# Kernel optimization log

Measured on AMD Instinct MI355X. Metric: run time of the kernel, lower is better.

The kernel has to match this reference:

```python
import jax, jax.numpy as jnp
import numpy as np
from jax import lax

B, C, H, W = 16, 256, 128, 128
MAX_ROOMS = 10

def _conv(x, w, b):
    y = lax.conv_general_dilated(x, w, window_strides=(1, 1), padding='SAME',
                                 dimension_numbers=('NCHW', 'OIHW', 'NCHW'))
    return y + b[None, :, None, None]

def setup_inputs() -> dict:
    key = jax.random.key(0)
    ks = jax.random.split(key, 16)
    def w(k, shape, fan_in):
        return jax.random.normal(k, shape, jnp.float32) * (1.0 / np.sqrt(fan_in))
    inp = {
        'features': jax.random.normal(ks[0], (B, C, H, W), jnp.float32),
        'conv1_w': w(ks[1], (C // 2, C, 3, 3), C * 9),
        'conv1_b': jnp.zeros((C // 2,), jnp.float32),
        'conv2_w': w(ks[2], (MAX_ROOMS, C // 2, 3, 3), (C // 2) * 9),
        'conv2_b': jnp.zeros((MAX_ROOMS,), jnp.float32),
        'lin1_w': w(ks[3], (256, C * 64), C * 64),
        'lin1_b': jnp.zeros((256,), jnp.float32),
        'lin2_w': w(ks[4], (128, 256), 256),
        'lin2_b': jnp.zeros((128,), jnp.float32),
        'adj1_w': w(ks[5], (64, 256), 256),
        'adj1_b': jnp.zeros((64,), jnp.float32),
        'adj2_w': w(ks[6], (32, 64), 64),
        'adj2_b': jnp.zeros((32,), jnp.float32),
        'adj3_w': w(ks[7], (1, 32), 32),
        'adj3_b': jnp.zeros((1,), jnp.float32),
    }
    return inp

def reference(features, conv1_w, conv1_b, conv2_w, conv2_b,
              lin1_w, lin1_b, lin2_w, lin2_b,
              adj1_w, adj1_b, adj2_w, adj2_b, adj3_w, adj3_b):
    # room detector: conv -> relu -> conv -> sigmoid
    h = jax.nn.relu(_conv(features, conv1_w, conv1_b))
    room_maps = jax.nn.sigmoid(_conv(h, conv2_w, conv2_b))  # [B, max_rooms, H, W]

    # room features: adaptive avg pool to 8x8 (exact since H,W divisible by 8)
    b, c = features.shape[0], features.shape[1]
    pooled = features.reshape(b, c, 8, H // 8, 8, W // 8).mean(axis=(3, 5))  # [B,C,8,8]
    flat = pooled.reshape(b, c * 64)
    feat = jax.nn.relu(flat @ lin1_w.T + lin1_b) @ lin2_w.T + lin2_b  # [B,128]

    # adjacency: original loop uses the SAME pair_feat=cat([feat,feat]) for every (i,j),
    # so compute one prob per batch row and broadcast to all off-diagonal entries.
    pair = jnp.concatenate([feat, feat], axis=-1)  # [B,256]
    a = jax.nn.relu(pair @ adj1_w.T + adj1_b)
    a = jax.nn.relu(a @ adj2_w.T + adj2_b)
    p = jax.nn.sigmoid(a @ adj3_w.T + adj3_b)  # [B,1]
    off_diag = 1.0 - jnp.eye(MAX_ROOMS, dtype=features.dtype)
    adjacency = p[:, :, None] * off_diag[None]  # [B, max_rooms, max_rooms]

    return room_maps, feat, adjacency
```

## Files before the change

### kernel.cpp

```cpp
#include <hip/hip_runtime.h>

#define HH 128
#define WW 128
#define FEAT_OFF 2621440ull
#define ADJ_OFF  2623488ull

typedef __bf16 bf16x8 __attribute__((ext_vector_type(8)));
typedef float  f32x4  __attribute__((ext_vector_type(4)));
typedef float  f32x16 __attribute__((ext_vector_type(16)));

__device__ __forceinline__ unsigned short f2bf(float f) {
  unsigned int u = __float_as_uint(f);
  unsigned int r = ((u >> 16) & 1u) + 0x7fffu;
  return (unsigned short)((u + r) >> 16);
}
__device__ __forceinline__ void gl_lds16(const void* g, void* l) {
  __builtin_amdgcn_global_load_lds((const __attribute__((address_space(1))) unsigned int*)g,
                                   (__attribute__((address_space(3))) unsigned int*)l, 16, 0, 0);
}
__device__ __forceinline__ int SW(int r) { return (r ^ (r >> 2)) & 3; }

#define FENCE() asm volatile("" ::: "memory")
#define BARRIER() do { FENCE(); __builtin_amdgcn_s_barrier(); FENCE(); } while (0)
#define LBAR() do { asm volatile("s_waitcnt lgkmcnt(0)" ::: "memory"); __builtin_amdgcn_s_barrier(); FENCE(); } while (0)

__global__ void prep_kernel(const float* __restrict__ w1, const float* __restrict__ w2,
                            unsigned short* __restrict__ W1t, unsigned short* __restrict__ W2t,
                            unsigned short* __restrict__ zp) {
  int id = blockIdx.x * 256 + threadIdx.x;
  if (id < 2048) zp[id] = 0;
  if (id < 294912) {
    int ci = id & 255, co = (id >> 8) & 127, dxy = id >> 15;
    int dy = dxy / 3, dx = dxy - 3 * dy;
    W1t[id] = f2bf(w1[((co * 256 + ci) * 3 + dy) * 3 + dx]);
  }
  if (id < 18432) {
    int ci = id & 127, co = (id >> 7) & 15, dxy = id >> 11;
    int dy = dxy / 3, dx = dxy - 3 * dy;
    W2t[id] = (co < 10) ? f2bf(w2[((co * 128 + ci) * 3 + dy) * 3 + dx]) : (unsigned short)0;
  }
}

__global__ void nhwc_kernel(const float* __restrict__ F, unsigned short* __restrict__ Xn,
                            float* __restrict__ part) {
  __shared__ __align__(16) unsigned short tile[16384];
  __shared__ float pl[1024];
  int t = threadIdx.x, bi = blockIdx.x;
  int chalf = bi & 1, y = (bi >> 1) & 127, b = bi >> 8;
  int c0 = chalf * 128;
  int cp = t >> 2, xq = t & 3;
  const float* rowA = F + (((size_t)(b * 256 + c0 + cp * 2)) * HH + y) * WW + xq * 32;
  const float* rowB = rowA + (size_t)HH * WW;
  unsigned int* tw = (unsigned int*)tile;
  float s00 = 0.f, s01 = 0.f, s10 = 0.f, s11 = 0.f;
#pragma unroll
  for (int jj = 0; jj < 8; ++jj) {
    float4 va = *(const float4*)(rowA + jj * 4);
    float4 vb = *(const float4*)(rowB + jj * 4);
    float av[4] = {va.x, va.y, va.z, va.w};
    float bv[4] = {vb.x, vb.y, vb.z, vb.w};
#pragma unroll
    for (int e = 0; e < 4; ++e) {
      int xl = jj * 4 + e;
      int x = xq * 32 + xl;
      if (xl < 16) { s00 += av[e]; s10 += bv[e]; } else { s01 += av[e]; s11 += bv[e]; }
      unsigned int word = (unsigned int)f2bf(av[e]) | ((unsigned int)f2bf(bv[e]) << 16);
      tw[x * 64 + (((cp >> 2) ^ (x & 15)) << 2) + (cp & 3)] = word;
    }
  }
  pl[(cp * 2 + 0) * 8 + xq * 2 + 0] = s00;
  pl[(cp * 2 + 0) * 8 + xq * 2 + 1] = s01;
  pl[(cp * 2 + 1) * 8 + xq * 2 + 0] = s10;
  pl[(cp * 2 + 1) * 8 + xq * 2 + 1] = s11;
  __syncthreads();
  int x = t >> 1, h = t & 1;
  unsigned short* dst = Xn + ((((size_t)b * HH + y) * WW) + x) * 256 + c0;
#pragma unroll
  for (int k = 0; k < 8; ++k) {
    int s = h * 8 + k;
    *(uint4*)(dst + s * 8) = *(const uint4*)(tile + x * 128 + ((s ^ (x & 15)) << 3));
  }
  *(float4*)&part[((((size_t)b * 128 + y) * 2) + chalf) * 1024 + t * 4] = *(const float4*)&pl[t * 4];
}

__global__ void pool3_kernel(const float* __restrict__ part, float* __restrict__ pooled) {
  int bi = blockIdx.x, t = threadIdx.x;
  int py = bi & 7, chalf = (bi >> 3) & 1, b = bi >> 4;
#pragma unroll
  for (int q = 0; q < 4; ++q) {
    int i = q * 256 + t;
    float s = 0.f;
#pragma unroll
    for (int yy = 0; yy < 16; ++yy)
      s += part[((((size_t)b * 128 + py * 16 + yy) * 2) + chalf) * 1024 + i];
    int ch = i >> 3, px = i & 7;
    pooled[(size_t)b * 16384 + (chalf * 128 + ch) * 64 + py * 8 + px] = s * (1.f / 256.f);
  }
}

__global__ __launch_bounds__(512) void conv1_kernel(const unsigned short* __restrict__ X,
                                                    const unsigned short* __restrict__ Wt,
                                                    const float* __restrict__ bias,
                                                    unsigned short* __restrict__ Hout,
                                                    const unsigned short* __restrict__ zp) {
  extern __shared__ __align__(16) unsigned short smem[];
  const int t = threadIdx.x, l = t & 63, w = t >> 6;
  int bid = (blockIdx.x & 7) * 64 + (blockIdx.x >> 3);
  const int b = bid >> 5, y0 = (bid & 31) * 4;
  const int lane31 = l & 31, lh = l >> 5;
  const int yloc = w >> 1, xh = w & 1, xoff = xh * 64;

  f32x16 acc[2][4];
#pragma unroll
  for (int i = 0; i < 2; ++i)
#pragma unroll
    for (int j = 0; j < 4; ++j)
#pragma unroll
      for (int e = 0; e < 16; ++e) acc[i][j][e] = 0.f;

  auto issue_group = [&](int p, int i0, int i1, int bufsel) {
    int dy = p >> 3, cb = p & 7;
    unsigned short* buf = smem + bufsel * 30720;
    for (int i = i0; i < i1; ++i) {
      int c = w + 8 * i;
      if (c >= 60) break;
      const unsigned short* g;
      if (c < 36) {
        int air = c / 9, jj = c - air * 9;
        int er = jj * 16 + (l >> 2);
        int xin = er - 1;
        int row = y0 - 1 + dy + air;
        if (row >= 0 && row < HH && xin >= 0 && xin < WW && er < 130) {
          int kq = (l & 3) ^ SW(er);
          g = X + (((size_t)b * HH + row) * WW + xin) * 256 + cb * 32 + kq * 8;
        } else g = zp + l * 8;
      } else {
        int cc = c - 36;
        int dxi = cc >> 3, jj = cc & 7;
        int co = jj * 16 + (l >> 2);
        int kq = (l & 3) ^ SW(co);
        g = Wt + (((size_t)(dy * 3 + dxi)) * 128 + co) * 256 + cb * 32 + kq * 8;
      }
      gl_lds16(g, buf + c * 512);
    }
  };

  issue_group(0, 0, 8, 0);

  for (int p = 0; p < 24; ++p) {
    const unsigned short* buf = smem + (p & 1) * 30720;
    const unsigned short* Ab = buf + yloc * 4608;
    const unsigned short* Bb = buf + 18432;
    const int nsel = (p + 1) & 1;

    if (p < 23) issue_group(p + 1, 0, 3, nsel);
    FENCE();
    if (p < 23) asm volatile("s_waitcnt vmcnt(3)" ::: "memory");
    else        asm volatile("s_waitcnt vmcnt(0)" ::: "memory");
    BARRIER();

#pragma unroll
    for (int dx = 0; dx < 3; ++dx) {
      if (p < 23) {
        if (dx == 1)      issue_group(p + 1, 3, 6, nsel);
        else if (dx == 2) issue_group(p + 1, 6, 8, nsel);
      }
      bf16x8 a[2][2], bb[4][2];
#pragma unroll
      for (int tm = 0; tm < 2; ++tm)
#pragma unroll
        for (int ks = 0; ks < 2; ++ks) {
          int er = xoff + tm * 32 + lane31 + dx;
          int slot = (ks * 2 + lh) ^ SW(er);
          a[tm][ks] = *(const bf16x8*)(Ab + er * 32 + slot * 8);
        }
#pragma unroll
      for (int tn = 0; tn < 4; ++tn)
#pragma unroll
        for (int ks = 0; ks < 2; ++ks) {
          int co = tn * 32 + lane31;
          int slot = (ks * 2 + lh) ^ SW(co);
          bb[tn][ks] = *(const bf16x8*)(Bb + dx * 4096 + co * 32 + slot * 8);
        }
      __builtin_amdgcn_s_setprio(1);
#pragma unroll
      for (int ks = 0; ks < 2; ++ks)
#pragma unroll
        for (int tm = 0; tm < 2; ++tm)
#pragma unroll
          for (int tn = 0; tn < 4; ++tn)
            acc[tm][tn] = __builtin_amdgcn_mfma_f32_32x32x16_bf16(a[tm][ks], bb[tn][ks], acc[tm][tn], 0, 0, 0);
      __builtin_amdgcn_s_setprio(0);
    }
    BARRIER();
  }

  unsigned short* E = smem;
  for (int r = 0; r < 2; ++r) {
    if (xh == r) {
#pragma unroll
      for (int tn = 0; tn < 4; ++tn) {
        int co = tn * 32 + lane31;
        float bv = bias[co];
#pragma unroll
        for (int tm = 0; tm < 2; ++tm)
#pragma unroll
          for (int rr = 0; rr < 16; ++rr) {
            int row = (rr & 3) + 8 * (rr >> 2) + 4 * lh;
            int xl = tm * 32 + row;
            E[yloc * 8704 + xl * 136 + co] = f2bf(fmaxf(acc[tm][tn][rr] + bv, 0.f));
          }
      }
    }
    LBAR();
#pragma unroll
    for (int k = 0; k < 8; ++k) {
      int idx = k * 512 + t;
      int yl = idx >> 10, rem = idx & 1023;
      int xl = rem >> 4, oct = rem & 15;
      const uint4 v = *(const uint4*)(E + yl * 8704 + xl * 136 + oct * 8);
      size_t g = (((size_t)b * HH + y0 + yl) * WW + r * 64 + xl) * 128 + oct * 8;
      *(uint4*)(Hout + g) = v;
    }
    LBAR();
  }
}

__global__ __launch_bounds__(256) void conv2_kernel(const unsigned short* __restrict__ Hn,
                                                    const unsigned short* __restrict__ Wt,
                                                    const float* __restrict__ bias,
                                                    float* __restrict__ rmaps,
                                                    const unsigned short* __restrict__ zp) {
  extern __shared__ __align__(16) unsigned short smem[];
  const int t = threadIdx.x, l = t & 63, w = t >> 6;
  int bid = (blockIdx.x & 7) * 64 + (blockIdx.x >> 3);
  const int b = bid >> 5, y0 = (bid & 31) * 4;
  const int ko = l >> 4, r0 = l & 15;
  const int yloc = w;

  f32x4 acc[8];
#pragma unroll
  for (int i = 0; i < 8; ++i) acc[i] = {0.f, 0.f, 0.f, 0.f};

  auto stage = [&](int cb, int bufsel) {
    unsigned short* buf = smem + bufsel * 32256;
    for (int c = w; c < 63; c += 4) {
      const unsigned short* g;
      if (c < 54) {
        int air = c / 9, jj = c - air * 9;
        int er = jj * 16 + (l >> 2);
        int xin = er - 1;
        int row = y0 - 1 + air;
        if (row >= 0 && row < HH && xin >= 0 && xin < WW && er < 130) {
          int kq = (l & 3) ^ SW(er);
          g = Hn + (((size_t)b * HH + row) * WW + xin) * 128 + cb * 32 + kq * 8;
        } else g = zp + l * 8;
      } else {
        int tap = c - 54;
        int co = l >> 2;
        int kq = (l & 3) ^ SW(co);
        g = Wt + ((size_t)tap * 16 + co) * 128 + cb * 32 + kq * 8;
      }
      gl_lds16(g, buf + c * 512);
    }
  };

  stage(0, 0);
  for (int p = 0; p < 4; ++p) {
    if (p < 3) {
      stage(p + 1, (p + 1) & 1);
      FENCE();
      asm volatile("s_waitcnt vmcnt(15)" ::: "memory");
    } else {
      FENCE();
      asm volatile("s_waitcnt vmcnt(0)" ::: "memory");
    }
    BARRIER();
    const unsigned short* buf = smem + (p & 1) * 32256;
#pragma unroll
    for (int dy = 0; dy < 3; ++dy) {
      const unsigned short* Ab = buf + (yloc + dy) * 4608;
#pragma unroll
      for (int dx = 0; dx < 3; ++dx) {
        int tap = dy * 3 + dx;
        bf16x8 bbf = *(const bf16x8*)(buf + (54 + tap) * 512 + r0 * 32 + ((ko ^ SW(r0)) << 3));
        __builtin_amdgcn_s_setprio(1);
#pragma unroll
        for (int mf = 0; mf < 8; ++mf) {
          int er = mf * 16 + r0 + dx;
          bf16x8 a = *(const bf16x8*)(Ab + er * 32 + ((ko ^ SW(er)) << 3));
          acc[mf] = __builtin_amdgcn_mfma_f32_16x16x32_bf16(a, bbf, acc[mf], 0, 0, 0);
        }
        __builtin_amdgcn_s_setprio(0);
      }
    }
    BARRIER();
  }

  int co = r0;
  if (co < 10) {
    float bv = bias[co];
    int y = y0 + yloc;
#pragma unroll
    for (int mf = 0; mf < 8; ++mf) {
      int x = mf * 16 + ko * 4;
      float4 o;
      o.x = 1.f / (1.f + __expf(-(acc[mf][0] + bv)));
      o.y = 1.f / (1.f + __expf(-(acc[mf][1] + bv)));
      o.z = 1.f / (1.f + __expf(-(acc[mf][2] + bv)));
      o.w = 1.f / (1.f + __expf(-(acc[mf][3] + bv)));
      *(float4*)&rmaps[(((size_t)b * 10 + co) * HH + y) * WW + x] = o;
    }
  }
}

__global__ void lin1_kernel(const float* __restrict__ pooled, const float* __restrict__ w1,
                            const float* __restrict__ b1, float* __restrict__ hidden) {
  int o = blockIdx.x, t = threadIdx.x;
  float acc[16];
#pragma unroll
  for (int b = 0; b < 16; ++b) acc[b] = 0.f;
  const float* wr = w1 + (size_t)o * 16384;
  for (int i = t; i < 16384; i += 256) {
    float wv = wr[i];
#pragma unroll
    for (int b = 0; b < 16; ++b) acc[b] += wv * pooled[(size_t)b * 16384 + i];
  }
  __shared__ float red[16][4];
#pragma unroll
  for (int b = 0; b < 16; ++b) {
    float v = acc[b];
    for (int s = 32; s; s >>= 1) v += __shfl_down(v, s);
    if ((t & 63) == 0) red[b][t >> 6] = v;
  }
  __syncthreads();
  if (t < 16) {
    float v = red[t][0] + red[t][1] + red[t][2] + red[t][3] + b1[o];
    hidden[o * 16 + t] = fmaxf(v, 0.f);
  }
}

__global__ void head_kernel(const float* __restrict__ hidden,
                            const float* __restrict__ w2, const float* __restrict__ b2,
                            const float* __restrict__ a1w, const float* __restrict__ a1b,
                            const float* __restrict__ a2w, const float* __restrict__ a2b,
                            const float* __restrict__ a3w, const float* __restrict__ a3b,
                            float* __restrict__ out) {
  int b = blockIdx.x, t = threadIdx.x;
  __shared__ float hid[256], fs[128], a1[64], a2[32], pv;
  hid[t] = hidden[t * 16 + b];
  __syncthreads();
  if (t < 128) {
    float s = b2[t];
    for (int k = 0; k < 256; ++k) s += hid[k] * w2[t * 256 + k];
    fs[t] = s;
    out[FEAT_OFF + b * 128 + t] = s;
  }
  __syncthreads();
  if (t < 64) {
    float s = a1b[t];
    for (int k = 0; k < 128; ++k) s += fs[k] * (a1w[t * 256 + k] + a1w[t * 256 + 128 + k]);
    a1[t] = fmaxf(s, 0.f);
  }
  __syncthreads();
  if (t < 32) {
    float s = a2b[t];
    for (int k = 0; k < 64; ++k) s += a1[k] * a2w[t * 64 + k];
    a2[t] = fmaxf(s, 0.f);
  }
  __syncthreads();
  if (t == 0) {
    float s = a3b[0];
    for (int k = 0; k < 32; ++k) s += a2[k] * a3w[k];
    pv = 1.f / (1.f + __expf(-s));
  }
  __syncthreads();
  if (t < 100) out[ADJ_OFF + b * 100 + t] = ((t / 10) == (t % 10)) ? 0.f : pv;
}

extern "C" void kernel_launch(void* const* d_in, const int* in_sizes, int n_in,
                              void* d_out, int out_size, void* d_ws, size_t ws_size,
                              hipStream_t stream) {
  const float* F   = (const float*)d_in[0];
  const float* w1  = (const float*)d_in[1];
  const float* b1  = (const float*)d_in[2];
  const float* w2  = (const float*)d_in[3];
  const float* b2  = (const float*)d_in[4];
  const float* l1w = (const float*)d_in[5];
  const float* l1b = (const float*)d_in[6];
  const float* l2w = (const float*)d_in[7];
  const float* l2b = (const float*)d_in[8];
  const float* a1w = (const float*)d_in[9];
  const float* a1b = (const float*)d_in[10];
  const float* a2w = (const float*)d_in[11];
  const float* a2b = (const float*)d_in[12];
  const float* a3w = (const float*)d_in[13];
  const float* a3b = (const float*)d_in[14];
  float* out = (float*)d_out;
  char* ws = (char*)d_ws;

  const size_t zp_off   = 0;
  const size_t w1t_off  = 4096;
  const size_t w2t_off  = w1t_off + 589824;
  const size_t xn_off   = w2t_off + 36864;
  const size_t hn_off   = xn_off + 134217728ull;
  const size_t pool_off = hn_off + 67108864ull;
  const size_t hid_off  = pool_off + 1048576ull;
  const size_t need     = hid_off + 16384ull;
  if (ws_size < need) return;

  unsigned short* zp  = (unsigned short*)(ws + zp_off);
  unsigned short* W1t = (unsigned short*)(ws + w1t_off);
  unsigned short* W2t = (unsigned short*)(ws + w2t_off);
  unsigned short* Xn  = (unsigned short*)(ws + xn_off);
  unsigned short* Hn  = (unsigned short*)(ws + hn_off);
  float* part   = (float*)(ws + hn_off);
  float* pooled = (float*)(ws + pool_off);
  float* hidden = (float*)(ws + hid_off);

  hipFuncSetAttribute((const void*)conv1_kernel, hipFuncAttributeMaxDynamicSharedMemorySize, 122880);
  hipFuncSetAttribute((const void*)conv2_kernel, hipFuncAttributeMaxDynamicSharedMemorySize, 129024);

  prep_kernel<<<1152, 256, 0, stream>>>(w1, w2, W1t, W2t, zp);
  nhwc_kernel<<<4096, 256, 0, stream>>>(F, Xn, part);
  pool3_kernel<<<256, 256, 0, stream>>>(part, pooled);
  conv1_kernel<<<512, 512, 122880, stream>>>(Xn, W1t, b1, Hn, zp);
  conv2_kernel<<<512, 256, 129024, stream>>>(Hn, W2t, b2, out, zp);
  lin1_kernel<<<256, 256, 0, stream>>>(pooled, l1w, l1b, hidden);
  head_kernel<<<16, 256, 0, stream>>>(hidden, l2w, l2b, a1w, a1b, a2w, a2b, a3w, a3b, out);
}
```

Baseline: 367.1 us.

## Fuse weight prep into NHWC kernel, transpose pooled for lin1, tweak conv2 waits

Folds the weight-conversion prep kernel into the first 1152 blocks of the NHWC transpose kernel, removing one launch. The pool kernel also writes a batch-minor transposed copy of the pooled features, so lin1 can read 16 batch values as contiguous float4 vectors and load the weights as float4. In conv2, the wait count is split per wave and the s_setprio hints around the MFMA loop are removed. This adds an extra pooled buffer write and puts prep work on a few transpose blocks, which may slightly unbalance them.

```diff
diff --git a/kernel.cpp b/kernel.cpp
--- a/kernel.cpp
+++ b/kernel.cpp
@@ -24,28 +24,28 @@
 #define BARRIER() do { FENCE(); __builtin_amdgcn_s_barrier(); FENCE(); } while (0)
 #define LBAR() do { asm volatile("s_waitcnt lgkmcnt(0)" ::: "memory"); __builtin_amdgcn_s_barrier(); FENCE(); } while (0)
 
-__global__ void prep_kernel(const float* __restrict__ w1, const float* __restrict__ w2,
+__global__ void nhwc_kernel(const float* __restrict__ F, unsigned short* __restrict__ Xn,
+                            float* __restrict__ part,
+                            const float* __restrict__ w1, const float* __restrict__ w2,
                             unsigned short* __restrict__ W1t, unsigned short* __restrict__ W2t,
                             unsigned short* __restrict__ zp) {
-  int id = blockIdx.x * 256 + threadIdx.x;
-  if (id < 2048) zp[id] = 0;
-  if (id < 294912) {
-    int ci = id & 255, co = (id >> 8) & 127, dxy = id >> 15;
-    int dy = dxy / 3, dx = dxy - 3 * dy;
-    W1t[id] = f2bf(w1[((co * 256 + ci) * 3 + dy) * 3 + dx]);
-  }
-  if (id < 18432) {
-    int ci = id & 127, co = (id >> 7) & 15, dxy = id >> 11;
-    int dy = dxy / 3, dx = dxy - 3 * dy;
-    W2t[id] = (co < 10) ? f2bf(w2[((co * 128 + ci) * 3 + dy) * 3 + dx]) : (unsigned short)0;
-  }
-}
-
-__global__ void nhwc_kernel(const float* __restrict__ F, unsigned short* __restrict__ Xn,
-                            float* __restrict__ part) {
   __shared__ __align__(16) unsigned short tile[16384];
   __shared__ float pl[1024];
   int t = threadIdx.x, bi = blockIdx.x;
+  if (bi < 1152) {
+    int id = bi * 256 + t;
+    if (id < 2048) zp[id] = 0;
+    if (id < 294912) {
+      int ci = id & 255, co = (id >> 8) & 127, dxy = id >> 15;
+      int dy = dxy / 3, dx = dxy - 3 * dy;
+      W1t[id] = f2bf(w1[((co * 256 + ci) * 3 + dy) * 3 + dx]);
+    }
+    if (id < 18432) {
+      int ci = id & 127, co = (id >> 7) & 15, dxy = id >> 11;
+      int dy = dxy / 3, dx = dxy - 3 * dy;
+      W2t[id] = (co < 10) ? f2bf(w2[((co * 128 + ci) * 3 + dy) * 3 + dx]) : (unsigned short)0;
+    }
+  }
   int chalf = bi & 1, y = (bi >> 1) & 127, b = bi >> 8;
   int c0 = chalf * 128;
   int cp = t >> 2, xq = t & 3;
@@ -83,7 +83,8 @@
   *(float4*)&part[((((size_t)b * 128 + y) * 2) + chalf) * 1024 + t * 4] = *(const float4*)&pl[t * 4];
 }
 
-__global__ void pool3_kernel(const float* __restrict__ part, float* __restrict__ pooled) {
+__global__ void pool3_kernel(const float* __restrict__ part, float* __restrict__ pooled,
+                             float* __restrict__ pooledT) {
   int bi = blockIdx.x, t = threadIdx.x;
   int py = bi & 7, chalf = (bi >> 3) & 1, b = bi >> 4;
 #pragma unroll
@@ -94,7 +95,10 @@
     for (int yy = 0; yy < 16; ++yy)
       s += part[((((size_t)b * 128 + py * 16 + yy) * 2) + chalf) * 1024 + i];
     int ch = i >> 3, px = i & 7;
-    pooled[(size_t)b * 16384 + (chalf * 128 + ch) * 64 + py * 8 + px] = s * (1.f / 256.f);
+    float v = s * (1.f / 256.f);
+    int flat = (chalf * 128 + ch) * 64 + py * 8 + px;
+    pooled[(size_t)b * 16384 + flat] = v;
+    pooledT[(size_t)flat * 16 + b] = v;
   }
 }
 
@@ -270,7 +274,8 @@
     if (p < 3) {
       stage(p + 1, (p + 1) & 1);
       FENCE();
-      asm volatile("s_waitcnt vmcnt(15)" ::: "memory");
+      if (w < 3) asm volatile("s_waitcnt vmcnt(16)" ::: "memory");
+      else       asm volatile("s_waitcnt vmcnt(15)" ::: "memory");
     } else {
       FENCE();
       asm volatile("s_waitcnt vmcnt(0)" ::: "memory");
@@ -284,14 +289,12 @@
       for (int dx = 0; dx < 3; ++dx) {
         int tap = dy * 3 + dx;
         bf16x8 bbf = *(const bf16x8*)(buf + (54 + tap) * 512 + r0 * 32 + ((ko ^ SW(r0)) << 3));
-        __builtin_amdgcn_s_setprio(1);
 #pragma unroll
         for (int mf = 0; mf < 8; ++mf) {
           int er = mf * 16 + r0 + dx;
           bf16x8 a = *(const bf16x8*)(Ab + er * 32 + ((ko ^ SW(er)) << 3));
           acc[mf] = __builtin_amdgcn_mfma_f32_16x16x32_bf16(a, bbf, acc[mf], 0, 0, 0);
         }
-        __builtin_amdgcn_s_setprio(0);
       }
     }
     BARRIER();
@@ -314,25 +317,36 @@
   }
 }
 
-__global__ void lin1_kernel(const float* __restrict__ pooled, const float* __restrict__ w1,
+__global__ void lin1_kernel(const float* __restrict__ pooledT, const float* __restrict__ w1,
                             const float* __restrict__ b1, float* __restrict__ hidden) {
   int o = blockIdx.x, t = threadIdx.x;
-  float acc[16];
-#pragma unroll
-  for (int b = 0; b < 16; ++b) acc[b] = 0.f;
+  f32x4 acc[4];
+#pragma unroll
+  for (int q = 0; q < 4; ++q) acc[q] = {0.f, 0.f, 0.f, 0.f};
   const float* wr = w1 + (size_t)o * 16384;
-  for (int i = t; i < 16384; i += 256) {
-    float wv = wr[i];
-#pragma unroll
-    for (int b = 0; b < 16; ++b) acc[b] += wv * pooled[(size_t)b * 16384 + i];
+  for (int i0 = t * 4; i0 < 16384; i0 += 1024) {
+    float4 wv = *(const float4*)&wr[i0];
+    float wa[4] = {wv.x, wv.y, wv.z, wv.w};
+#pragma unroll
+    for (int j = 0; j < 4; ++j) {
+      const float* pt = pooledT + (size_t)(i0 + j) * 16;
+#pragma unroll
+      for (int q = 0; q < 4; ++q) {
+        f32x4 pv = *(const f32x4*)(pt + q * 4);
+#pragma unroll
+        for (int e = 0; e < 4; ++e) acc[q][e] += wa[j] * pv[e];
+      }
+    }
   }
   __shared__ float red[16][4];
 #pragma unroll
-  for (int b = 0; b < 16; ++b) {
-    float v = acc[b];
-    for (int s = 32; s; s >>= 1) v += __shfl_down(v, s);
-    if ((t & 63) == 0) red[b][t >> 6] = v;
-  }
+  for (int q = 0; q < 4; ++q)
+#pragma unroll
+    for (int e = 0; e < 4; ++e) {
+      float v = acc[q][e];
+      for (int s = 32; s; s >>= 1) v += __shfl_down(v, s);
+      if ((t & 63) == 0) red[q * 4 + e][t >> 6] = v;
+    }
   __syncthreads();
   if (t < 16) {
     float v = red[t][0] + red[t][1] + red[t][2] + red[t][3] + b1[o];
@@ -405,7 +419,8 @@
   const size_t xn_off   = w2t_off + 36864;
   const size_t hn_off   = xn_off + 134217728ull;
   const size_t pool_off = hn_off + 67108864ull;
-  const size_t hid_off  = pool_off + 1048576ull;
+  const size_t poolT_off= pool_off + 1048576ull;
+  const size_t hid_off  = poolT_off + 1048576ull;
   const size_t need     = hid_off + 16384ull;
   if (ws_size < need) return;
 
@@ -414,18 +429,19 @@
   unsigned short* W2t = (unsigned short*)(ws + w2t_off);
   unsigned short* Xn  = (unsigned short*)(ws + xn_off);
   unsigned short* Hn  = (unsigned short*)(ws + hn_off);
-  float* part   = (float*)(ws + hn_off);
-  float* pooled = (float*)(ws + pool_off);
-  float* hidden = (float*)(ws + hid_off);
+  float* part    = (float*)(ws + hn_off);
+  float* pooled  = (float*)(ws + pool_off);
+  float* pooledT = (float*)(ws + poolT_off);
+  float* hidden  = (float*)(ws + hid_off);
+  (void)pooled;
 
   hipFuncSetAttribute((const void*)conv1_kernel, hipFuncAttributeMaxDynamicSharedMemorySize, 122880);
   hipFuncSetAttribute((const void*)conv2_kernel, hipFuncAttributeMaxDynamicSharedMemorySize, 129024);
 
-  prep_kernel<<<1152, 256, 0, stream>>>(w1, w2, W1t, W2t, zp);
-  nhwc_kernel<<<4096, 256, 0, stream>>>(F, Xn, part);
-  pool3_kernel<<<256, 256, 0, stream>>>(part, pooled);
+  nhwc_kernel<<<4096, 256, 0, stream>>>(F, Xn, part, w1, w2, W1t, W2t, zp);
+  pool3_kernel<<<256, 256, 0, stream>>>(part, pooled, pooledT);
   conv1_kernel<<<512, 512, 122880, stream>>>(Xn, W1t, b1, Hn, zp);
   conv2_kernel<<<512, 256, 129024, stream>>>(Hn, W2t, b2, out, zp);
-  lin1_kernel<<<256, 256, 0, stream>>>(pooled, l1w, l1b, hidden);
+  lin1_kernel<<<256, 256, 0, stream>>>(pooledT, l1w, l1b, hidden);
   head_kernel<<<16, 256, 0, stream>>>(hidden, l2w, l2b, a1w, a1b, a2w, a2b, a3w, a3b, out);
 }
```

After: 340.2 us. -7.3%, faster.
